# Kernel optimization log

Measured on AMD Instinct MI355X. Metric: run time of the kernel, lower is better.

The kernel has to match this reference:

```python
import jax, jax.numpy as jnp
import numpy as np

U, I, R, E, K, D, RD, OUT = 100000, 50000, 5, 100000, 4, 16, 64, 64
KF = 2      # selected factor index (self.k)
TAU = 0.5   # contrastive temperature


def setup_inputs() -> dict:
    key = jax.random.key(0)
    ks = jax.random.split(key, 17)
    inp = {
        'user_h': jax.random.normal(ks[0], (R, U, D), jnp.float32),
        'item_h': jax.random.normal(ks[1], (R, I, D), jnp.float32),
        'user_hsum': jax.random.normal(ks[2], (R, U, K, D), jnp.float32) * 0.25,
        'item_hsum': jax.random.normal(ks[3], (R, I, K, D), jnp.float32) * 0.25,
        'review_feat': jax.random.normal(ks[4], (R, E, K, RD), jnp.float32) * 0.2,
        'prototypes': jax.random.normal(ks[5], (K, RD), jnp.float32) * 0.2,
        'eta': jax.random.normal(ks[6], (R, E), jnp.float32),
        'node_w_fwd': jax.random.normal(ks[7], (R, D, D), jnp.float32) / np.sqrt(D),
        'node_w_rev': jax.random.normal(ks[8], (R, D, D), jnp.float32) / np.sqrt(D),
        'review_w_fwd': jax.random.normal(ks[9], (R, RD, D), jnp.float32) / np.sqrt(RD),
        'review_w_rev': jax.random.normal(ks[10], (R, RD, D), jnp.float32) / np.sqrt(RD),
        'ufc_w': jax.random.normal(ks[11], (D, OUT), jnp.float32) / np.sqrt(D),
        'ufc_b': jnp.zeros((OUT,), jnp.float32),
        'ifc_w': jax.random.normal(ks[12], (D, OUT), jnp.float32) / np.sqrt(D),
        'ifc_b': jnp.zeros((OUT,), jnp.float32),
        'rows': jax.random.randint(ks[13], (R, E), 0, U),
        'cols': jax.random.randint(ks[14], (R, E), 0, I),
    }
    return inp


def _l2n(x):
    return x / jnp.linalg.norm(x, axis=-1, keepdims=True)


def reference(user_h, item_h, user_hsum, item_hsum, review_feat, prototypes, eta,
              node_w_fwd, node_w_rev, review_w_fwd, review_w_rev,
              ufc_w, ufc_b, ifc_w, ifc_b, rows, cols):
    # --- per-rating contrastive edge scores (fwd and rev etypes are symmetric) ---
    ead_list = []
    norm_u = jnp.zeros((U,), user_h.dtype)
    norm_i = jnp.zeros((I,), user_h.dtype)
    for r in range(R):
        row, col = rows[r], cols[r]
        # factor-KF node similarity (L2-normalized feats)
        ru = _l2n(user_h[r])[row]               # [E, D]
        ri = _l2n(item_h[r])[col]               # [E, D]
        sim_k = jnp.sum(ru * ri, -1) / TAU      # [E]
        sim_all = jnp.sum(user_hsum[r][row] * item_hsum[r][col], -1) / TAU  # [E, K]
        exp_sim = jnp.exp(sim_k) / jnp.sum(jnp.exp(sim_all), -1)
        # prototype anchor scores on review features
        rf_k = review_feat[r, :, KF, :]                      # [E, RD]
        ad_k = (rf_k @ prototypes[KF]) / TAU                 # [E]
        ad_all = jnp.sum(review_feat[r] * prototypes, -1) / TAU  # [E, K]
        ead = jnp.exp(ad_k) / jnp.sum(jnp.exp(ad_all), -1)
        # sigmoid-gated combine with per-edge eta
        g = jax.nn.sigmoid(eta[r])
        ead = g * ead + (1.0 - g) * exp_sim
        ead_list.append(ead)
        # scatter-sum normalization; fwd+rev each contribute once, then /2 in torch
        norm_u = norm_u + jax.ops.segment_sum(ead, row, num_segments=U)
        norm_i = norm_i + jax.ops.segment_sum(ead, col, num_segments=I)
    # --- normalized edge weights + weighted message passing (HeteroGraphConv sum) ---
    ufeat = jnp.zeros((U, D), user_h.dtype)
    ifeat = jnp.zeros((I, D), user_h.dtype)
    int_dist = []
    for r in range(R):
        row, col = rows[r], cols[r]
        w = ead_list[r] / jnp.sqrt(norm_u[row] * norm_i[col])  # [E]
        int_dist.append(w[:, None])                            # item-side etype weights
        rf_k = review_feat[r, :, KF, :]
        # user -> item messages
        m_fwd = ((user_h[r] @ node_w_fwd[r])[row] + rf_k @ review_w_fwd[r]) * w[:, None]
        ifeat = ifeat + jax.ops.segment_sum(m_fwd, col, num_segments=I)
        # item -> user messages (rev etype, same review feats and weights)
        m_rev = ((item_h[r] @ node_w_rev[r])[col] + rf_k @ review_w_rev[r]) * w[:, None]
        ufeat = ufeat + jax.ops.segment_sum(m_rev, row, num_segments=U)
    int_dist = jnp.concatenate(int_dist, axis=0)  # [R*E, 1]
    leaky = lambda x: jnp.where(x >= 0, x, 0.1 * x)
    ufeat = leaky(ufeat) @ ufc_w + ufc_b
    ifeat = leaky(ifeat) @ ifc_w + ifc_b
    return ufeat, ifeat, int_dist
```

## Files before the change

### kernel.cpp

```cpp
#include <hip/hip_runtime.h>
#include <cstddef>

#define DEV_INLINE __device__ __forceinline__

constexpr int U_N = 100000;
constexpr int I_N = 50000;
constexpr int R_N = 5;
constexpr int E_N = 100000;
constexpr int K_N = 4;
constexpr int D_N = 16;
constexpr int RD_N = 64;
constexpr int OUT_N = 64;
constexpr int KF_N = 2;
constexpr float INV_TAU = 2.0f;

constexpr int NE_TOT = R_N * E_N;
constexpr int NNODE  = U_N + I_N;
constexpr int NB_SCAN = (NNODE + 255) / 256;

constexpr size_t OFS_CNT    = 0;
constexpr size_t OFS_OFF    = 150000;
constexpr size_t OFS_BSUMS  = 300016;
constexpr size_t OFS_CURSOR = 301040;
constexpr size_t OFS_LIST   = 451040;
constexpr size_t OFS_EAD    = 1451040;
constexpr size_t OFS_NORM   = 1951040;
constexpr size_t OFS_MFWD   = 2101040;
constexpr size_t OFS_MREV   = 10101040;
constexpr size_t OFS_UFEAT  = 18101040;
constexpr size_t OFS_IFEAT  = 19701040;

DEV_INLINE float dot4(float4 a, float4 b) { return a.x*b.x + a.y*b.y + a.z*b.z + a.w*b.w; }
DEV_INLINE void fma4(float4& a, float s, float4 w) { a.x += s*w.x; a.y += s*w.y; a.z += s*w.z; a.w += s*w.w; }
DEV_INLINE float comp(float4 v, int i) { return i == 0 ? v.x : i == 1 ? v.y : i == 2 ? v.z : v.w; }

__global__ __launch_bounds__(256) void count_kernel(
    const int* __restrict__ rows, const int* __restrict__ cols, int* __restrict__ cnt)
{
    const int idx = blockIdx.x * 256 + threadIdx.x;
    if (idx >= NE_TOT) return;
    atomicAdd(cnt + rows[idx], 1);
    atomicAdd(cnt + U_N + cols[idx], 1);
}

__global__ __launch_bounds__(256) void scan1_kernel(
    const int* __restrict__ cnt, int* __restrict__ off, int* __restrict__ bsums)
{
    __shared__ int s[256];
    const int t = threadIdx.x;
    const int i = blockIdx.x * 256 + t;
    const int v = (i < NNODE) ? cnt[i] : 0;
    s[t] = v;
    __syncthreads();
#pragma unroll
    for (int d = 1; d < 256; d <<= 1) {
        const int x = (t >= d) ? s[t - d] : 0;
        __syncthreads();
        s[t] += x;
        __syncthreads();
    }
    if (i < NNODE) off[i] = s[t] - v;
    if (t == 255) bsums[blockIdx.x] = s[255];
}

__global__ __launch_bounds__(1024) void scan2_kernel(int* __restrict__ bsums)
{
    __shared__ int s[1024];
    const int t = threadIdx.x;
    const int v = (t < NB_SCAN) ? bsums[t] : 0;
    s[t] = v;
    __syncthreads();
#pragma unroll
    for (int d = 1; d < 1024; d <<= 1) {
        const int x = (t >= d) ? s[t - d] : 0;
        __syncthreads();
        s[t] += x;
        __syncthreads();
    }
    if (t < NB_SCAN) bsums[t] = s[t] - v;
}

__global__ __launch_bounds__(256) void scan3_kernel(
    int* __restrict__ off, const int* __restrict__ bsums, int* __restrict__ cursor)
{
    const int i = blockIdx.x * 256 + threadIdx.x;
    if (i < NNODE) {
        const int v = off[i] + bsums[i >> 8];
        off[i] = v;
        cursor[i] = v;
    }
    if (i == 0) off[NNODE] = 2 * NE_TOT;
}

__global__ __launch_bounds__(256) void fill_kernel(
    const int* __restrict__ rows, const int* __restrict__ cols,
    int* __restrict__ cursor, int* __restrict__ list)
{
    const int idx = blockIdx.x * 256 + threadIdx.x;
    if (idx >= NE_TOT) return;
    const int p = atomicAdd(cursor + rows[idx], 1);
    list[p] = idx;
    const int q = atomicAdd(cursor + U_N + cols[idx], 1);
    list[q] = idx;
}

__global__ __launch_bounds__(256) void phase1_kernel(
    const float* __restrict__ user_h, const float* __restrict__ item_h,
    const float* __restrict__ user_hsum, const float* __restrict__ item_hsum,
    const float* __restrict__ review_feat, const float* __restrict__ prototypes,
    const float* __restrict__ eta,
    const int* __restrict__ rows, const int* __restrict__ cols,
    float* __restrict__ ead_ws)
{
    __shared__ __align__(16) float proto_s[K_N * RD_N];
    const int tid = threadIdx.x;
    proto_s[tid] = prototypes[tid];
    __syncthreads();

    const int r = blockIdx.y;
    const int e = blockIdx.x * 64 + (tid >> 2);
    const int l = tid & 3;
    if (e >= E_N) return;
    const size_t re = (size_t)r * E_N + e;
    const int row = rows[re];
    const int col = cols[re];

    const float4* uh4 = (const float4*)(user_h + ((size_t)r * U_N + row) * D_N);
    const float4* ih4 = (const float4*)(item_h + ((size_t)r * I_N + col) * D_N);
    const float4 a = uh4[l], b = ih4[l];
    float du = dot4(a, a), di = dot4(b, b), dui = dot4(a, b);
    du  += __shfl_xor(du, 1);  du  += __shfl_xor(du, 2);
    di  += __shfl_xor(di, 1);  di  += __shfl_xor(di, 2);
    dui += __shfl_xor(dui, 1); dui += __shfl_xor(dui, 2);
    const float sim_k = dui / sqrtf(du * di) * INV_TAU;

    const float4* us4 = (const float4*)(user_hsum + ((size_t)r * U_N + row) * (K_N * D_N)) + l * 4;
    const float4* is4 = (const float4*)(item_hsum + ((size_t)r * I_N + col) * (K_N * D_N)) + l * 4;
    float s = 0.f;
#pragma unroll
    for (int q = 0; q < 4; ++q) s += dot4(us4[q], is4[q]);
    float ssum = expf(s * INV_TAU);
    ssum += __shfl_xor(ssum, 1); ssum += __shfl_xor(ssum, 2);
    const float exp_sim = expf(sim_k) / ssum;

    const float4* rf4 = (const float4*)(review_feat + re * (size_t)(K_N * RD_N)) + l * 16;
    const float4* pr4 = (const float4*)proto_s + l * 16;
    float t = 0.f;
#pragma unroll
    for (int q = 0; q < 16; ++q) t += dot4(rf4[q], pr4[q]);
    t *= INV_TAU;
    float adsum = expf(t);
    adsum += __shfl_xor(adsum, 1); adsum += __shfl_xor(adsum, 2);
    const float adk = __shfl(t, KF_N, 4);
    const float ead_rev = expf(adk) / adsum;

    const float g = 1.0f / (1.0f + expf(-eta[re]));
    const float ead = g * ead_rev + (1.0f - g) * exp_sim;
    if (l == 0) ead_ws[re] = ead;
}

__global__ __launch_bounds__(256) void norm_kernel(
    const int* __restrict__ off, const int* __restrict__ list,
    const float* __restrict__ ead, float* __restrict__ norm)
{
    const int n = blockIdx.x * 256 + threadIdx.x;
    if (n >= NNODE) return;
    const int p0 = off[n], p1 = off[n + 1];
    float acc = 0.f;
    for (int p = p0; p < p1; ++p) acc += ead[list[p]];
    norm[n] = acc;
}

__global__ __launch_bounds__(256) void phase2_kernel(
    const float* __restrict__ user_h, const float* __restrict__ item_h,
    const float* __restrict__ review_feat,
    const float* __restrict__ node_w_fwd, const float* __restrict__ node_w_rev,
    const float* __restrict__ review_w_fwd, const float* __restrict__ review_w_rev,
    const int* __restrict__ rows, const int* __restrict__ cols,
    const float* __restrict__ norm, const float* __restrict__ ead_ws,
    float* __restrict__ m_fwd, float* __restrict__ m_rev,
    float* __restrict__ int_dist)
{
    __shared__ __align__(16) float nwf_s[D_N * D_N];
    __shared__ __align__(16) float nwr_s[D_N * D_N];
    __shared__ __align__(16) float rwf_s[RD_N * D_N];
    __shared__ __align__(16) float rwr_s[RD_N * D_N];
    const int tid = threadIdx.x;
    const int r = blockIdx.y;
    nwf_s[tid] = node_w_fwd[r * D_N * D_N + tid];
    nwr_s[tid] = node_w_rev[r * D_N * D_N + tid];
#pragma unroll
    for (int q = 0; q < 4; ++q) {
        rwf_s[q*256 + tid] = review_w_fwd[r * RD_N * D_N + q*256 + tid];
        rwr_s[q*256 + tid] = review_w_rev[r * RD_N * D_N + q*256 + tid];
    }
    __syncthreads();

    const int e = blockIdx.x * 256 + tid;
    if (e >= E_N) return;
    const size_t re = (size_t)r * E_N + e;
    const int row = rows[re];
    const int col = cols[re];

    const float w = ead_ws[re] / sqrtf(norm[row] * norm[U_N + col]);
    int_dist[re] = w;

    float4 mf[4], mr[4];
#pragma unroll
    for (int q = 0; q < 4; ++q) {
        mf[q] = make_float4(0.f, 0.f, 0.f, 0.f);
        mr[q] = make_float4(0.f, 0.f, 0.f, 0.f);
    }

    const float4* uh4 = (const float4*)(user_h + ((size_t)r * U_N + row) * D_N);
    const float4* ih4 = (const float4*)(item_h + ((size_t)r * I_N + col) * D_N);
    const float4* nf4 = (const float4*)nwf_s;
    const float4* nr4 = (const float4*)nwr_s;
#pragma unroll
    for (int jq = 0; jq < 4; ++jq) {
        float4 uv = uh4[jq], iv = ih4[jq];
#pragma unroll
        for (int jj = 0; jj < 4; ++jj) {
            const int j = jq*4 + jj;
            const float uu = comp(uv, jj);
            const float ii = comp(iv, jj);
#pragma unroll
            for (int q = 0; q < 4; ++q) {
                fma4(mf[q], uu, nf4[j*4 + q]);
                fma4(mr[q], ii, nr4[j*4 + q]);
            }
        }
    }

    const float4* rfk4 = (const float4*)(review_feat + re * (size_t)(K_N * RD_N) + KF_N * RD_N);
    const float4* rf4w = (const float4*)rwf_s;
    const float4* rr4w = (const float4*)rwr_s;
#pragma unroll
    for (int jq = 0; jq < 16; ++jq) {
        float4 v4 = rfk4[jq];
#pragma unroll
        for (int jj = 0; jj < 4; ++jj) {
            const int j = jq*4 + jj;
            const float v = comp(v4, jj);
#pragma unroll
            for (int q = 0; q < 4; ++q) {
                fma4(mf[q], v, rf4w[j*4 + q]);
                fma4(mr[q], v, rr4w[j*4 + q]);
            }
        }
    }

    float4* mfp = (float4*)(m_fwd + re * (size_t)D_N);
    float4* mrp = (float4*)(m_rev + re * (size_t)D_N);
#pragma unroll
    for (int q = 0; q < 4; ++q) {
        float4 f = mf[q], g2 = mr[q];
        f.x *= w; f.y *= w; f.z *= w; f.w *= w;
        g2.x *= w; g2.y *= w; g2.z *= w; g2.w *= w;
        mfp[q] = f;
        mrp[q] = g2;
    }
}

__global__ __launch_bounds__(256) void gather_kernel(
    const int* __restrict__ off, const int* __restrict__ list,
    const float* __restrict__ m_fwd, const float* __restrict__ m_rev,
    float* __restrict__ ufeat, float* __restrict__ ifeat)
{
    const int gid = blockIdx.x * 256 + threadIdx.x;
    const int n = gid >> 2;
    const int l = gid & 3;
    if (n >= NNODE) return;
    const int p0 = off[n], p1 = off[n + 1];
    const float* __restrict__ src = (n < U_N) ? m_rev : m_fwd;
    float4 acc = make_float4(0.f, 0.f, 0.f, 0.f);
    for (int p = p0; p < p1; ++p) {
        const float4 v = *((const float4*)(src + (size_t)list[p] * D_N) + l);
        acc.x += v.x; acc.y += v.y; acc.z += v.z; acc.w += v.w;
    }
    float* dst = (n < U_N) ? (ufeat + (size_t)n * D_N) : (ifeat + (size_t)(n - U_N) * D_N);
    *((float4*)dst + l) = acc;
}

__global__ __launch_bounds__(256) void fc_kernel(
    const float* __restrict__ acc, const float* __restrict__ W,
    const float* __restrict__ bias, float* __restrict__ out, int n)
{
    __shared__ __align__(16) float w_s[D_N * OUT_N];
    __shared__ __align__(16) float b_s[OUT_N];
    const int tid = threadIdx.x;
#pragma unroll
    for (int q = 0; q < 4; ++q) w_s[q*256 + tid] = W[q*256 + tid];
    if (tid < OUT_N) b_s[tid] = bias[tid];
    __syncthreads();

    const int gid = blockIdx.x * 256 + tid;
    if (gid >= n * (OUT_N / 4)) return;
    const int u  = gid >> 4;
    const int oc = (gid & 15) * 4;

    const float4* a4 = (const float4*)(acc + (size_t)u * D_N);
    float4 s = *(const float4*)(b_s + oc);
#pragma unroll
    for (int dq = 0; dq < 4; ++dq) {
        float4 av = a4[dq];
#pragma unroll
        for (int jj = 0; jj < 4; ++jj) {
            const int d = dq*4 + jj;
            float x = comp(av, jj);
            x = (x >= 0.f) ? x : 0.1f * x;
            fma4(s, x, *(const float4*)(w_s + d*OUT_N + oc));
        }
    }
    *((float4*)(out + (size_t)u * OUT_N + oc)) = s;
}

extern "C" void kernel_launch(void* const* d_in, const int* in_sizes, int n_in,
                              void* d_out, int out_size, void* d_ws, size_t ws_size,
                              hipStream_t stream)
{
    const float* user_h       = (const float*)d_in[0];
    const float* item_h       = (const float*)d_in[1];
    const float* user_hsum    = (const float*)d_in[2];
    const float* item_hsum    = (const float*)d_in[3];
    const float* review_feat  = (const float*)d_in[4];
    const float* prototypes   = (const float*)d_in[5];
    const float* eta          = (const float*)d_in[6];
    const float* node_w_fwd   = (const float*)d_in[7];
    const float* node_w_rev   = (const float*)d_in[8];
    const float* review_w_fwd = (const float*)d_in[9];
    const float* review_w_rev = (const float*)d_in[10];
    const float* ufc_w        = (const float*)d_in[11];
    const float* ufc_b        = (const float*)d_in[12];
    const float* ifc_w        = (const float*)d_in[13];
    const float* ifc_b        = (const float*)d_in[14];
    const int*   rows         = (const int*)d_in[15];
    const int*   cols         = (const int*)d_in[16];

    int*   wsi = (int*)d_ws;
    float* wsf = (float*)d_ws;
    float* out = (float*)d_out;

    int*   cnt    = wsi + OFS_CNT;
    int*   off    = wsi + OFS_OFF;
    int*   bsums  = wsi + OFS_BSUMS;
    int*   cursor = wsi + OFS_CURSOR;
    int*   list   = wsi + OFS_LIST;
    float* ead    = wsf + OFS_EAD;
    float* norm   = wsf + OFS_NORM;
    float* m_fwd  = wsf + OFS_MFWD;
    float* m_rev  = wsf + OFS_MREV;
    float* ufeat  = wsf + OFS_UFEAT;
    float* ifeat  = wsf + OFS_IFEAT;

    hipMemsetAsync(cnt, 0, NNODE * sizeof(int), stream);

    const dim3 blk(256);
    const dim3 g_e((NE_TOT + 255) / 256);

    count_kernel<<<g_e, blk, 0, stream>>>(rows, cols, cnt);
    scan1_kernel<<<dim3(NB_SCAN), blk, 0, stream>>>(cnt, off, bsums);
    scan2_kernel<<<dim3(1), dim3(1024), 0, stream>>>(bsums);
    scan3_kernel<<<dim3((NNODE + 255) / 256), blk, 0, stream>>>(off, bsums, cursor);
    fill_kernel<<<g_e, blk, 0, stream>>>(rows, cols, cursor, list);

    phase1_kernel<<<dim3((E_N * 4 + 255) / 256, R_N), blk, 0, stream>>>(
        user_h, item_h, user_hsum, item_hsum, review_feat, prototypes, eta,
        rows, cols, ead);

    norm_kernel<<<dim3((NNODE + 255) / 256), blk, 0, stream>>>(off, list, ead, norm);

    float* int_dist_out = out + (size_t)U_N * OUT_N + (size_t)I_N * OUT_N;
    phase2_kernel<<<dim3((E_N + 255) / 256, R_N), blk, 0, stream>>>(
        user_h, item_h, review_feat,
        node_w_fwd, node_w_rev, review_w_fwd, review_w_rev, rows, cols,
        norm, ead, m_fwd, m_rev, int_dist_out);

    gather_kernel<<<dim3((NNODE * 4 + 255) / 256), blk, 0, stream>>>(
        off, list, m_fwd, m_rev, ufeat, ifeat);

    fc_kernel<<<dim3((U_N * (OUT_N/4) + 255) / 256), blk, 0, stream>>>(
        ufeat, ufc_w, ufc_b, out, U_N);
    fc_kernel<<<dim3((I_N * (OUT_N/4) + 255) / 256), blk, 0, stream>>>(
        ifeat, ifc_w, ifc_b, out + (size_t)U_N * OUT_N, I_N);
}
```

Baseline: 1.144 ms.

## Fuse message computation into phase1 and gather with FC, unweighted messages

Message projections (node and review linear maps) move into phase1, which already loads user_h, item_h and review features, so the separate phase2 pass that re-gathered them is gone. Messages are stored unweighted, and the normalized edge weight is applied during the per-node gather, computed by a light wscale kernel that writes int_dist. The gather is fused with LeakyReLU and the output FC, removing the ufeat/ifeat round trip and two kernel launches. The cost is extra LDS and register pressure in phase1 and one extra weight load per edge in the gather.

New measurement: 1.083 ms. 1.06x faster.

```diff
diff --git a/kernel.cpp b/kernel.cpp
--- a/kernel.cpp
+++ b/kernel.cpp
@@ -27,8 +27,6 @@
 constexpr size_t OFS_NORM   = 1951040;
 constexpr size_t OFS_MFWD   = 2101040;
 constexpr size_t OFS_MREV   = 10101040;
-constexpr size_t OFS_UFEAT  = 18101040;
-constexpr size_t OFS_IFEAT  = 19701040;
 
 DEV_INLINE float dot4(float4 a, float4 b) { return a.x*b.x + a.y*b.y + a.z*b.z + a.w*b.w; }
 DEV_INLINE void fma4(float4& a, float s, float4 w) { a.x += s*w.x; a.y += s*w.y; a.z += s*w.z; a.w += s*w.w; }
@@ -109,15 +107,29 @@
     const float* __restrict__ user_hsum, const float* __restrict__ item_hsum,
     const float* __restrict__ review_feat, const float* __restrict__ prototypes,
     const float* __restrict__ eta,
+    const float* __restrict__ node_w_fwd, const float* __restrict__ node_w_rev,
+    const float* __restrict__ review_w_fwd, const float* __restrict__ review_w_rev,
     const int* __restrict__ rows, const int* __restrict__ cols,
-    float* __restrict__ ead_ws)
+    float* __restrict__ ead_ws,
+    float* __restrict__ m_fwd, float* __restrict__ m_rev)
 {
     __shared__ __align__(16) float proto_s[K_N * RD_N];
+    __shared__ __align__(16) float nwf_s[D_N * D_N];
+    __shared__ __align__(16) float nwr_s[D_N * D_N];
+    __shared__ __align__(16) float rwf_s[RD_N * D_N];
+    __shared__ __align__(16) float rwr_s[RD_N * D_N];
     const int tid = threadIdx.x;
+    const int r = blockIdx.y;
     proto_s[tid] = prototypes[tid];
+    nwf_s[tid] = node_w_fwd[r * D_N * D_N + tid];
+    nwr_s[tid] = node_w_rev[r * D_N * D_N + tid];
+#pragma unroll
+    for (int q = 0; q < 4; ++q) {
+        rwf_s[q*256 + tid] = review_w_fwd[r * RD_N * D_N + q*256 + tid];
+        rwr_s[q*256 + tid] = review_w_rev[r * RD_N * D_N + q*256 + tid];
+    }
     __syncthreads();
 
-    const int r = blockIdx.y;
     const int e = blockIdx.x * 64 + (tid >> 2);
     const int l = tid & 3;
     if (e >= E_N) return;
@@ -157,6 +169,37 @@
     const float g = 1.0f / (1.0f + expf(-eta[re]));
     const float ead = g * ead_rev + (1.0f - g) * exp_sim;
     if (l == 0) ead_ws[re] = ead;
+
+    float4 mf = make_float4(0.f, 0.f, 0.f, 0.f);
+    float4 mr = make_float4(0.f, 0.f, 0.f, 0.f);
+    const float4* nf4 = (const float4*)nwf_s;
+    const float4* nr4 = (const float4*)nwr_s;
+#pragma unroll
+    for (int jq = 0; jq < 4; ++jq) {
+        const float4 uv = uh4[jq];
+        const float4 iv = ih4[jq];
+#pragma unroll
+        for (int jj = 0; jj < 4; ++jj) {
+            const int j = jq*4 + jj;
+            fma4(mf, comp(uv, jj), nf4[j*4 + l]);
+            fma4(mr, comp(iv, jj), nr4[j*4 + l]);
+        }
+    }
+    const float4* rfk4 = (const float4*)(review_feat + re * (size_t)(K_N * RD_N) + KF_N * RD_N);
+    const float4* rf4w = (const float4*)rwf_s;
+    const float4* rr4w = (const float4*)rwr_s;
+#pragma unroll
+    for (int jq = 0; jq < 16; ++jq) {
+        const float4 v4 = rfk4[jq];
+#pragma unroll
+        for (int jj = 0; jj < 4; ++jj) {
+            const int j = jq*4 + jj;
+            fma4(mf, comp(v4, jj), rf4w[j*4 + l]);
+            fma4(mr, comp(v4, jj), rr4w[j*4 + l]);
+        }
+    }
+    *((float4*)(m_fwd + re * (size_t)D_N) + l) = mf;
+    *((float4*)(m_rev + re * (size_t)D_N) + l) = mr;
 }
 
 __global__ __launch_bounds__(256) void norm_kernel(
@@ -171,148 +214,89 @@
     norm[n] = acc;
 }
 
-__global__ __launch_bounds__(256) void phase2_kernel(
-    const float* __restrict__ user_h, const float* __restrict__ item_h,
-    const float* __restrict__ review_feat,
-    const float* __restrict__ node_w_fwd, const float* __restrict__ node_w_rev,
-    const float* __restrict__ review_w_fwd, const float* __restrict__ review_w_rev,
+__global__ __launch_bounds__(256) void wscale_kernel(
     const int* __restrict__ rows, const int* __restrict__ cols,
-    const float* __restrict__ norm, const float* __restrict__ ead_ws,
-    float* __restrict__ m_fwd, float* __restrict__ m_rev,
-    float* __restrict__ int_dist)
-{
-    __shared__ __align__(16) float nwf_s[D_N * D_N];
-    __shared__ __align__(16) float nwr_s[D_N * D_N];
-    __shared__ __align__(16) float rwf_s[RD_N * D_N];
-    __shared__ __align__(16) float rwr_s[RD_N * D_N];
-    const int tid = threadIdx.x;
-    const int r = blockIdx.y;
-    nwf_s[tid] = node_w_fwd[r * D_N * D_N + tid];
-    nwr_s[tid] = node_w_rev[r * D_N * D_N + tid];
-#pragma unroll
-    for (int q = 0; q < 4; ++q) {
-        rwf_s[q*256 + tid] = review_w_fwd[r * RD_N * D_N + q*256 + tid];
-        rwr_s[q*256 + tid] = review_w_rev[r * RD_N * D_N + q*256 + tid];
-    }
-    __syncthreads();
-
-    const int e = blockIdx.x * 256 + tid;
-    if (e >= E_N) return;
-    const size_t re = (size_t)r * E_N + e;
-    const int row = rows[re];
-    const int col = cols[re];
-
-    const float w = ead_ws[re] / sqrtf(norm[row] * norm[U_N + col]);
-    int_dist[re] = w;
-
-    float4 mf[4], mr[4];
-#pragma unroll
-    for (int q = 0; q < 4; ++q) {
-        mf[q] = make_float4(0.f, 0.f, 0.f, 0.f);
-        mr[q] = make_float4(0.f, 0.f, 0.f, 0.f);
-    }
-
-    const float4* uh4 = (const float4*)(user_h + ((size_t)r * U_N + row) * D_N);
-    const float4* ih4 = (const float4*)(item_h + ((size_t)r * I_N + col) * D_N);
-    const float4* nf4 = (const float4*)nwf_s;
-    const float4* nr4 = (const float4*)nwr_s;
-#pragma unroll
-    for (int jq = 0; jq < 4; ++jq) {
-        float4 uv = uh4[jq], iv = ih4[jq];
-#pragma unroll
-        for (int jj = 0; jj < 4; ++jj) {
-            const int j = jq*4 + jj;
-            const float uu = comp(uv, jj);
-            const float ii = comp(iv, jj);
-#pragma unroll
-            for (int q = 0; q < 4; ++q) {
-                fma4(mf[q], uu, nf4[j*4 + q]);
-                fma4(mr[q], ii, nr4[j*4 + q]);
-            }
-        }
-    }
-
-    const float4* rfk4 = (const float4*)(review_feat + re * (size_t)(K_N * RD_N) + KF_N * RD_N);
-    const float4* rf4w = (const float4*)rwf_s;
-    const float4* rr4w = (const float4*)rwr_s;
-#pragma unroll
-    for (int jq = 0; jq < 16; ++jq) {
-        float4 v4 = rfk4[jq];
-#pragma unroll
-        for (int jj = 0; jj < 4; ++jj) {
-            const int j = jq*4 + jj;
-            const float v = comp(v4, jj);
-#pragma unroll
-            for (int q = 0; q < 4; ++q) {
-                fma4(mf[q], v, rf4w[j*4 + q]);
-                fma4(mr[q], v, rr4w[j*4 + q]);
-            }
-        }
-    }
-
-    float4* mfp = (float4*)(m_fwd + re * (size_t)D_N);
-    float4* mrp = (float4*)(m_rev + re * (size_t)D_N);
-#pragma unroll
-    for (int q = 0; q < 4; ++q) {
-        float4 f = mf[q], g2 = mr[q];
-        f.x *= w; f.y *= w; f.z *= w; f.w *= w;
-        g2.x *= w; g2.y *= w; g2.z *= w; g2.w *= w;
-        mfp[q] = f;
-        mrp[q] = g2;
-    }
-}
-
-__global__ __launch_bounds__(256) void gather_kernel(
+    const float* __restrict__ ead, const float* __restrict__ norm,
+    float* __restrict__ w_out)
+{
+    const int idx = blockIdx.x * 256 + threadIdx.x;
+    if (idx >= NE_TOT) return;
+    const float nu = norm[rows[idx]];
+    const float ni = norm[U_N + cols[idx]];
+    w_out[idx] = ead[idx] / sqrtf(nu * ni);
+}
+
+__global__ __launch_bounds__(256) void gatherfc_kernel(
     const int* __restrict__ off, const int* __restrict__ list,
     const float* __restrict__ m_fwd, const float* __restrict__ m_rev,
-    float* __restrict__ ufeat, float* __restrict__ ifeat)
-{
-    const int gid = blockIdx.x * 256 + threadIdx.x;
+    const float* __restrict__ w_edge,
+    const float* __restrict__ ufc_w, const float* __restrict__ ufc_b,
+    const float* __restrict__ ifc_w, const float* __restrict__ ifc_b,
+    float* __restrict__ out)
+{
+    __shared__ __align__(16) float uw_s[D_N * OUT_N];
+    __shared__ __align__(16) float iw_s[D_N * OUT_N];
+    __shared__ __align__(16) float ub_s[OUT_N];
+    __shared__ __align__(16) float ib_s[OUT_N];
+    const int tid = threadIdx.x;
+#pragma unroll
+    for (int q = 0; q < 4; ++q) {
+        uw_s[q*256 + tid] = ufc_w[q*256 + tid];
+        iw_s[q*256 + tid] = ifc_w[q*256 + tid];
+    }
+    if (tid < OUT_N) ub_s[tid] = ufc_b[tid];
+    else if (tid < 2*OUT_N) ib_s[tid - OUT_N] = ifc_b[tid - OUT_N];
+    __syncthreads();
+
+    const int gid = blockIdx.x * 256 + tid;
     const int n = gid >> 2;
     const int l = gid & 3;
     if (n >= NNODE) return;
     const int p0 = off[n], p1 = off[n + 1];
-    const float* __restrict__ src = (n < U_N) ? m_rev : m_fwd;
+    const bool isU = (n < U_N);
+    const float* __restrict__ src = isU ? m_rev : m_fwd;
     float4 acc = make_float4(0.f, 0.f, 0.f, 0.f);
     for (int p = p0; p < p1; ++p) {
-        const float4 v = *((const float4*)(src + (size_t)list[p] * D_N) + l);
-        acc.x += v.x; acc.y += v.y; acc.z += v.z; acc.w += v.w;
-    }
-    float* dst = (n < U_N) ? (ufeat + (size_t)n * D_N) : (ifeat + (size_t)(n - U_N) * D_N);
-    *((float4*)dst + l) = acc;
-}
-
-__global__ __launch_bounds__(256) void fc_kernel(
-    const float* __restrict__ acc, const float* __restrict__ W,
-    const float* __restrict__ bias, float* __restrict__ out, int n)
-{
-    __shared__ __align__(16) float w_s[D_N * OUT_N];
-    __shared__ __align__(16) float b_s[OUT_N];
-    const int tid = threadIdx.x;
-#pragma unroll
-    for (int q = 0; q < 4; ++q) w_s[q*256 + tid] = W[q*256 + tid];
-    if (tid < OUT_N) b_s[tid] = bias[tid];
-    __syncthreads();
-
-    const int gid = blockIdx.x * 256 + tid;
-    if (gid >= n * (OUT_N / 4)) return;
-    const int u  = gid >> 4;
-    const int oc = (gid & 15) * 4;
-
-    const float4* a4 = (const float4*)(acc + (size_t)u * D_N);
-    float4 s = *(const float4*)(b_s + oc);
-#pragma unroll
-    for (int dq = 0; dq < 4; ++dq) {
-        float4 av = a4[dq];
+        const int e = list[p];
+        const float w = w_edge[e];
+        const float4 v = *((const float4*)(src + (size_t)e * D_N) + l);
+        fma4(acc, w, v);
+    }
+    acc.x = (acc.x >= 0.f) ? acc.x : 0.1f * acc.x;
+    acc.y = (acc.y >= 0.f) ? acc.y : 0.1f * acc.y;
+    acc.z = (acc.z >= 0.f) ? acc.z : 0.1f * acc.z;
+    acc.w = (acc.w >= 0.f) ? acc.w : 0.1f * acc.w;
+
+    const float* __restrict__ W = isU ? uw_s : iw_s;
+    const float* __restrict__ B = isU ? ub_s : ib_s;
+    float* __restrict__ dst = isU ? (out + (size_t)n * OUT_N)
+                                  : (out + (size_t)U_N * OUT_N + (size_t)(n - U_N) * OUT_N);
+
+    float4 s0 = *(const float4*)(B + 16*l + 0);
+    float4 s1 = *(const float4*)(B + 16*l + 4);
+    float4 s2 = *(const float4*)(B + 16*l + 8);
+    float4 s3 = *(const float4*)(B + 16*l + 12);
+#pragma unroll
+    for (int sl = 0; sl < 4; ++sl) {
+        float4 fv;
+        fv.x = __shfl(acc.x, sl, 4);
+        fv.y = __shfl(acc.y, sl, 4);
+        fv.z = __shfl(acc.z, sl, 4);
+        fv.w = __shfl(acc.w, sl, 4);
 #pragma unroll
         for (int jj = 0; jj < 4; ++jj) {
-            const int d = dq*4 + jj;
-            float x = comp(av, jj);
-            x = (x >= 0.f) ? x : 0.1f * x;
-            fma4(s, x, *(const float4*)(w_s + d*OUT_N + oc));
+            const int d = sl*4 + jj;
+            const float x = comp(fv, jj);
+            fma4(s0, x, *(const float4*)(W + d*OUT_N + 16*l + 0));
+            fma4(s1, x, *(const float4*)(W + d*OUT_N + 16*l + 4));
+            fma4(s2, x, *(const float4*)(W + d*OUT_N + 16*l + 8));
+            fma4(s3, x, *(const float4*)(W + d*OUT_N + 16*l + 12));
         }
     }
-    *((float4*)(out + (size_t)u * OUT_N + oc)) = s;
+    ((float4*)dst)[4*l + 0] = s0;
+    ((float4*)dst)[4*l + 1] = s1;
+    ((float4*)dst)[4*l + 2] = s2;
+    ((float4*)dst)[4*l + 3] = s3;
 }
 
 extern "C" void kernel_launch(void* const* d_in, const int* in_sizes, int n_in,
@@ -350,8 +334,6 @@
     float* norm   = wsf + OFS_NORM;
     float* m_fwd  = wsf + OFS_MFWD;
     float* m_rev  = wsf + OFS_MREV;
-    float* ufeat  = wsf + OFS_UFEAT;
-    float* ifeat  = wsf + OFS_IFEAT;
 
     hipMemsetAsync(cnt, 0, NNODE * sizeof(int), stream);
 
@@ -366,21 +348,15 @@
 
     phase1_kernel<<<dim3((E_N * 4 + 255) / 256, R_N), blk, 0, stream>>>(
         user_h, item_h, user_hsum, item_hsum, review_feat, prototypes, eta,
-        rows, cols, ead);
+        node_w_fwd, node_w_rev, review_w_fwd, review_w_rev,
+        rows, cols, ead, m_fwd, m_rev);
 
     norm_kernel<<<dim3((NNODE + 255) / 256), blk, 0, stream>>>(off, list, ead, norm);
 
     float* int_dist_out = out + (size_t)U_N * OUT_N + (size_t)I_N * OUT_N;
-    phase2_kernel<<<dim3((E_N + 255) / 256, R_N), blk, 0, stream>>>(
-        user_h, item_h, review_feat,
-        node_w_fwd, node_w_rev, review_w_fwd, review_w_rev, rows, cols,
-        norm, ead, m_fwd, m_rev, int_dist_out);
-
-    gather_kernel<<<dim3((NNODE * 4 + 255) / 256), blk, 0, stream>>>(
-        off, list, m_fwd, m_rev, ufeat, ifeat);
-
-    fc_kernel<<<dim3((U_N * (OUT_N/4) + 255) / 256), blk, 0, stream>>>(
-        ufeat, ufc_w, ufc_b, out, U_N);
-    fc_kernel<<<dim3((I_N * (OUT_N/4) + 255) / 256), blk, 0, stream>>>(
-        ifeat, ifc_w, ifc_b, out + (size_t)U_N * OUT_N, I_N);
-}
+    wscale_kernel<<<g_e, blk, 0, stream>>>(rows, cols, ead, norm, int_dist_out);
+
+    gatherfc_kernel<<<dim3((NNODE * 4 + 255) / 256), blk, 0, stream>>>(
+        off, list, m_fwd, m_rev, int_dist_out,
+        ufc_w, ufc_b, ifc_w, ifc_b, out);
+}
```
